# Kernel optimization log

Hardware: AMD Instinct MI355X
Metric: run time of the kernel (lower is better)

Reference implementation:

```python
import jax, jax.numpy as jnp
import numpy as np

B, N, C, H = 8, 784, 768, 16
HEAD_DIM = C // H
SCALE = HEAD_DIM ** -0.5


def rel_indices(num_patches):
    # ConViT relative position features: (dx, dy, dx^2+dy^2) per patch pair
    s = int(num_patches ** 0.5)
    ind = (jnp.arange(s)[None, :] - jnp.arange(s)[:, None]).astype(jnp.float32)
    indx = jnp.tile(ind, (s, s))                               # [N, N]
    indy = jnp.repeat(jnp.repeat(ind, s, axis=0), s, axis=1)   # [N, N]
    indd = indx ** 2 + indy ** 2
    return jnp.stack([indx, indy, indd], axis=-1)              # [N, N, 3]


def setup_inputs() -> dict:
    key = jax.random.key(0)
    ks = jax.random.split(key, 6)
    std = 0.02
    return {
        "x": jax.random.normal(ks[0], (B, N, C), dtype=jnp.float32),
        "Wq": jax.random.normal(ks[1], (C, C), dtype=jnp.float32) * std,
        "Wk": jax.random.normal(ks[2], (C, C), dtype=jnp.float32) * std,
        "Wv": jax.random.normal(ks[3], (C, C), dtype=jnp.float32) * std,
        "Wproj": jax.random.normal(ks[4], (C, C), dtype=jnp.float32) * std,
        "b_proj": jnp.zeros((C,), dtype=jnp.float32),
        "W_pos": jax.random.normal(ks[5], (H, 3), dtype=jnp.float32) * std,
        "b_pos": jnp.zeros((H,), dtype=jnp.float32),
        "gating": jnp.ones((H,), dtype=jnp.float32),
    }


def reference(x, Wq, Wk, Wv, Wproj, b_proj, W_pos, b_pos, gating):
    b, n, c = x.shape
    h, d = H, c // H

    def heads(W):
        # torch Linear: y = x @ W.T ; reshape to [b, h, n, d]
        return (x @ W.T).reshape(b, n, h, d).transpose(0, 2, 1, 3)

    q, k, v = heads(Wq), heads(Wk), heads(Wv)

    # content score: [b, h, n, n]
    patch_score = jnp.einsum('bhnd,bhmd->bhnm', q, k) * SCALE
    patch_score = jax.nn.softmax(patch_score, axis=-1)

    # positional score: rel [n,n,3] -> [h,n,n], broadcast over batch
    rel = rel_indices(n)
    pos_score = jnp.einsum('nmc,hc->hnm', rel, W_pos) + b_pos[:, None, None]
    pos_score = jax.nn.softmax(pos_score, axis=-1)

    g = jax.nn.sigmoid(gating)[None, :, None, None]  # [1,h,1,1]
    attn = (1.0 - g) * patch_score + g * pos_score[None]
    attn = attn / jnp.sum(attn, axis=-1, keepdims=True)

    out = jnp.einsum('bhnm,bhmd->bhnd', attn, v)
    out = out.transpose(0, 2, 1, 3).reshape(b, n, c)
    out = out @ Wproj.T + b_proj
    return out, attn, v
```

## Files before the change

### kernel.cpp

```cpp
#include <hip/hip_runtime.h>
#include <math.h>

#define BB 8
#define NN 784
#define CC 768
#define HH 16
#define DD 48
#define SCALE 0.14433756729740643f

#define ATTN_OFF ((size_t)BB*NN*CC)
#define V_OFF (ATTN_OFF + (size_t)BB*HH*NN*NN)

#define WS_XB ((size_t)0)
#define WS_WB ((size_t)4816896)
#define WS_QB (WS_WB + (size_t)4*589824)
#define WS_KB (WS_QB + (size_t)4816896)
#define WS_VT (WS_KB + (size_t)4816896)
#define WS_OB (WS_VT + (size_t)4816896)

using bf16x8 = __attribute__((ext_vector_type(8))) short;
using f32x4  = __attribute__((ext_vector_type(4))) float;

__device__ __forceinline__ short f2bf(float f) {
    union { float f; unsigned u; } uf; uf.f = f;
    unsigned u = uf.u;
    return (short)((u + 0x7FFFu + ((u >> 16) & 1u)) >> 16);
}
__device__ __forceinline__ bf16x8 bzero() {
    bf16x8 z = {0,0,0,0,0,0,0,0};
    return z;
}
__device__ __forceinline__ bf16x8 cvt8(float4 a, float4 b) {
    bf16x8 r;
    r[0]=f2bf(a.x); r[1]=f2bf(a.y); r[2]=f2bf(a.z); r[3]=f2bf(a.w);
    r[4]=f2bf(b.x); r[5]=f2bf(b.y); r[6]=f2bf(b.z); r[7]=f2bf(b.w);
    return r;
}
#define MFMA16(a,b,c) __builtin_amdgcn_mfma_f32_16x16x32_bf16((a),(b),(c),0,0,0)

__global__ __launch_bounds__(256) void cast_kernel(
    const float* __restrict__ x, const float* __restrict__ Wq,
    const float* __restrict__ Wk, const float* __restrict__ Wv,
    const float* __restrict__ Wp, short* __restrict__ xb, short* __restrict__ wb)
{
    int idx = blockIdx.x * 256 + threadIdx.x;
    const float* src;
    short* dst;
    if (idx < 1204224) {
        src = x + (size_t)idx * 4;
        dst = xb + (size_t)idx * 4;
    } else {
        int j = idx - 1204224;
        int sel = j / 147456;
        size_t off = (size_t)(j % 147456) * 4;
        const float* W = (sel == 0) ? Wq : (sel == 1) ? Wk : (sel == 2) ? Wv : Wp;
        src = W + off;
        dst = wb + (size_t)sel * 589824 + off;
    }
    float4 v = *(const float4*)src;
    union { short s[4]; uint2 u; } o;
    o.s[0] = f2bf(v.x); o.s[1] = f2bf(v.y); o.s[2] = f2bf(v.z); o.s[3] = f2bf(v.w);
    *(uint2*)dst = o.u;
}

__global__ __launch_bounds__(256) void qkv_mfma(
    const short* __restrict__ xb, const short* __restrict__ wb,
    short* __restrict__ qb, short* __restrict__ kb,
    float* __restrict__ vo, short* __restrict__ vt)
{
    const int t = threadIdx.x, l = t & 63, ww = t >> 6;
    const int quad = l >> 4, lc = l & 15;
    const int m0 = blockIdx.x * 128 + (ww >> 1) * 64;
    const int bn = blockIdx.y;
    const int wsel = bn / 6;
    const int colbase = (bn % 6) * 128 + (ww & 1) * 64;
    const short* W = wb + (size_t)wsel * 589824;

    f32x4 acc[4][4] = {};
    const short* arow = xb + (size_t)(m0 + lc) * 768 + quad * 8;
    const short* brow = W  + (size_t)(colbase + lc) * 768 + quad * 8;

    for (int k0 = 0; k0 < 768; k0 += 32) {
        bf16x8 af[4], bf[4];
#pragma unroll
        for (int i = 0; i < 4; i++) af[i] = *(const bf16x8*)(arow + (size_t)i * 16 * 768 + k0);
#pragma unroll
        for (int j = 0; j < 4; j++) bf[j] = *(const bf16x8*)(brow + (size_t)j * 16 * 768 + k0);
#pragma unroll
        for (int i = 0; i < 4; i++)
#pragma unroll
            for (int j = 0; j < 4; j++)
                acc[i][j] = MFMA16(af[i], bf[j], acc[i][j]);
    }

#pragma unroll
    for (int i = 0; i < 4; i++) {
#pragma unroll
        for (int j = 0; j < 4; j++) {
            const int o = colbase + j * 16 + lc;
            const int h = o / DD, d = o % DD;
#pragma unroll
            for (int r = 0; r < 4; r++) {
                const int m = m0 + i * 16 + quad * 4 + r;
                const int b = m / NN, n = m % NN;
                const size_t bhnd = (((size_t)b * HH + h) * NN + n) * DD + d;
                const float v = acc[i][j][r];
                if (wsel == 0)      qb[bhnd] = f2bf(v);
                else if (wsel == 1) kb[bhnd] = f2bf(v);
                else {
                    __builtin_nontemporal_store(v, vo + bhnd);
                    vt[((size_t)(b * HH + h) * DD + d) * NN + n] = f2bf(v);
                }
            }
        }
    }
}

__global__ __launch_bounds__(256) void attn_pv_fused(
    const short* __restrict__ qb, const short* __restrict__ kb,
    const short* __restrict__ vt,
    const float* __restrict__ W_pos, const float* __restrict__ b_pos,
    const float* __restrict__ gating, float* __restrict__ attn,
    short* __restrict__ ob)
{
    const int t = threadIdx.x, l = t & 63, ww = t >> 6;
    const int quad = l >> 4, lc = l & 15;
    const int bh = blockIdx.y, b = bh >> 4, h = bh & 15;
    const int row0 = blockIdx.x * 16;

    __shared__ __align__(16) float Sbuf[16][812];
    __shared__ float lxs[55], lys[55], fxs[55], fys[55];
    __shared__ float pmws[16][4];

    Sbuf[t >> 4][784 + (t & 15)] = 0.f;

    const short* qrow = qb + ((size_t)bh * NN + row0 + lc) * DD;
    bf16x8 qf0 = *(const bf16x8*)(qrow + quad * 8);
    bf16x8 qf1 = (quad < 2) ? *(const bf16x8*)(qrow + 32 + quad * 8) : bzero();

    float pmax[4] = {-3e38f, -3e38f, -3e38f, -3e38f};
    {
        int ct = ww;
        const short* krow = kb + ((size_t)bh * NN + ct * 16 + lc) * DD;
        bf16x8 kf0 = *(const bf16x8*)(krow + quad * 8);
        bf16x8 kf1 = (quad < 2) ? *(const bf16x8*)(krow + 32 + quad * 8) : bzero();
        while (ct < 49) {
            const int nct = ct + 4;
            bf16x8 nk0 = bzero(), nk1 = bzero();
            if (nct < 49) {
                const short* nrow = kb + ((size_t)bh * NN + nct * 16 + lc) * DD;
                nk0 = *(const bf16x8*)(nrow + quad * 8);
                nk1 = (quad < 2) ? *(const bf16x8*)(nrow + 32 + quad * 8) : bzero();
            }
            f32x4 cc = {0.f, 0.f, 0.f, 0.f};
            cc = MFMA16(qf0, kf0, cc);
            cc = MFMA16(qf1, kf1, cc);
            const int c0 = ct * 16;
#pragma unroll
            for (int r = 0; r < 4; r++) {
                Sbuf[quad * 4 + r][c0 + lc] = cc[r] * SCALE;
                pmax[r] = fmaxf(pmax[r], cc[r]);
            }
            kf0 = nk0; kf1 = nk1; ct = nct;
        }
    }
#pragma unroll
    for (int r = 0; r < 4; r++) {
        float v = pmax[r];
        v = fmaxf(v, __shfl_xor(v, 1));
        v = fmaxf(v, __shfl_xor(v, 2));
        v = fmaxf(v, __shfl_xor(v, 4));
        v = fmaxf(v, __shfl_xor(v, 8));
        if (lc == 0) pmws[quad * 4 + r][ww] = v;
    }

    const float w0 = W_pos[h * 3], w1 = W_pos[h * 3 + 1], w2 = W_pos[h * 3 + 2];
    if (t < 55) {
        const float d = (float)(t - 27);
        lxs[t] = fmaf(w2, d * d, w0 * d);
    } else if (t >= 64 && t < 119) {
        const float d = (float)(t - 91);
        lys[t - 64] = fmaf(w2, d * d, w1 * d);
    }

    __syncthreads();

    if (t < 55) {
        float m = lxs[0];
#pragma unroll
        for (int i = 1; i < 55; i++) m = fmaxf(m, lxs[i]);
        fxs[t] = __expf(lxs[t] - m);
    } else if (t >= 64 && t < 119) {
        float m = lys[0];
#pragma unroll
        for (int i = 1; i < 55; i++) m = fmaxf(m, lys[i]);
        fys[t - 64] = __expf(lys[t - 64] - m);
    }

    const int r = t >> 4, c = t & 15;
    const int nrow = row0 + r;
    const int nx = nrow % 28, ny = nrow / 28;

    const float sm = SCALE * fmaxf(fmaxf(pmws[r][0], pmws[r][1]),
                                   fmaxf(pmws[r][2], pmws[r][3]));
    float se = 0.f;
#pragma unroll 7
    for (int s = 0; s < 49; s++) {
        const float e = __expf(Sbuf[r][c + 16 * s] - sm);
        Sbuf[r][c + 16 * s] = e;
        se += e;
    }
    se += __shfl_xor(se, 1);
    se += __shfl_xor(se, 2);
    se += __shfl_xor(se, 4);
    se += __shfl_xor(se, 8);
    const float inv = 1.f / se;
    const float g = 1.f / (1.f + __expf(-gating[h]));

    __syncthreads();

    float Sx = 0.f, Sy = 0.f;
#pragma unroll
    for (int mx = 0; mx < 28; mx++) Sx += fxs[mx - nx + 27];
#pragma unroll
    for (int my = 0; my < 28; my++) Sy += fys[my - ny + 27];
    const float ginv = (1.f - g) * inv;
    const float gp = g / (Sx * Sy);

    float* arow = attn + ((size_t)bh * NN + nrow) * NN;
    {
        int mx = c, my = 0;
#pragma unroll 7
        for (int s = 0; s < 49; s++) {
            const int m = c + 16 * s;
            const float a = fmaf(Sbuf[r][m], ginv,
                                 fxs[mx - nx + 27] * fys[my - ny + 27] * gp);
            Sbuf[r][m] = a;
            __builtin_nontemporal_store(a, arow + m);
            mx += 16;
            if (mx >= 28) { mx -= 28; my++; }
        }
    }

    __syncthreads();

    const short* vbase = vt + (size_t)bh * DD * NN;
    f32x4 acc[3] = {};
    {
        const int kt0 = ww * 6;
        const int kt1 = (ww == 3) ? 25 : kt0 + 6;
        for (int kt = kt0; kt < kt1; kt++) {
            const int k0 = kt * 32 + quad * 8;
            float4 a0 = *(const float4*)&Sbuf[lc][k0];
            float4 a1 = *(const float4*)&Sbuf[lc][k0 + 4];
            bf16x8 af = cvt8(a0, a1);
#pragma unroll
            for (int j = 0; j < 3; j++) {
                bf16x8 bf = (k0 < NN)
                    ? *(const bf16x8*)(vbase + (size_t)(j * 16 + lc) * NN + k0)
                    : bzero();
                acc[j] = MFMA16(af, bf, acc[j]);
            }
        }
    }

    __syncthreads();

    float* Pacc = &Sbuf[0][0];
    if (ww > 0) {
#pragma unroll
        for (int j = 0; j < 3; j++)
            *(f32x4*)&Pacc[(((ww - 1) * 3 + j) * 64 + l) * 4] = acc[j];
    }

    __syncthreads();

    if (ww == 0) {
#pragma unroll
        for (int j = 0; j < 3; j++) {
#pragma unroll
            for (int w = 0; w < 3; w++)
                acc[j] += *(const f32x4*)&Pacc[((w * 3 + j) * 64 + l) * 4];
            const int d = h * DD + j * 16 + lc;
#pragma unroll
            for (int rr = 0; rr < 4; rr++) {
                const int rowi = row0 + quad * 4 + rr;
                ob[((size_t)b * NN + rowi) * CC + d] = f2bf(acc[j][rr]);
            }
        }
    }
}

__global__ __launch_bounds__(256) void proj_mfma(
    const short* __restrict__ ob, const short* __restrict__ wb,
    const float* __restrict__ bias, float* __restrict__ out)
{
    const int t = threadIdx.x, l = t & 63, ww = t >> 6;
    const int quad = l >> 4, lc = l & 15;
    const int m0 = blockIdx.x * 128 + (ww >> 1) * 64;
    const int colbase = blockIdx.y * 128 + (ww & 1) * 64;
    const short* W = wb + (size_t)3 * 589824;

    f32x4 acc[4][4] = {};
    const short* arow = ob + (size_t)(m0 + lc) * 768 + quad * 8;
    const short* brow = W  + (size_t)(colbase + lc) * 768 + quad * 8;

    for (int k0 = 0; k0 < 768; k0 += 32) {
        bf16x8 af[4], bf[4];
#pragma unroll
        for (int i = 0; i < 4; i++) af[i] = *(const bf16x8*)(arow + (size_t)i * 16 * 768 + k0);
#pragma unroll
        for (int j = 0; j < 4; j++) bf[j] = *(const bf16x8*)(brow + (size_t)j * 16 * 768 + k0);
#pragma unroll
        for (int i = 0; i < 4; i++)
#pragma unroll
            for (int j = 0; j < 4; j++)
                acc[i][j] = MFMA16(af[i], bf[j], acc[i][j]);
    }

#pragma unroll
    for (int i = 0; i < 4; i++) {
#pragma unroll
        for (int j = 0; j < 4; j++) {
            const int o = colbase + j * 16 + lc;
            const float bo = bias[o];
#pragma unroll
            for (int r = 0; r < 4; r++) {
                const int m = m0 + i * 16 + quad * 4 + r;
                __builtin_nontemporal_store(acc[i][j][r] + bo, out + (size_t)m * CC + o);
            }
        }
    }
}

extern "C" void kernel_launch(void* const* d_in, const int* in_sizes, int n_in,
                              void* d_out, int out_size, void* d_ws, size_t ws_size,
                              hipStream_t stream)
{
    const float* x      = (const float*)d_in[0];
    const float* Wq     = (const float*)d_in[1];
    const float* Wk     = (const float*)d_in[2];
    const float* Wv     = (const float*)d_in[3];
    const float* Wproj  = (const float*)d_in[4];
    const float* b_proj = (const float*)d_in[5];
    const float* W_pos  = (const float*)d_in[6];
    const float* b_pos  = (const float*)d_in[7];
    const float* gating = (const float*)d_in[8];

    float* out  = (float*)d_out;
    short* ws   = (short*)d_ws;

    short* xb = ws + WS_XB;
    short* wb = ws + WS_WB;
    short* qb = ws + WS_QB;
    short* kb = ws + WS_KB;
    short* vt = ws + WS_VT;
    short* ob = ws + WS_OB;
    float* attn = out + ATTN_OFF;
    float* vout = out + V_OFF;

    hipLaunchKernelGGL(cast_kernel, dim3(7008), dim3(256), 0, stream,
                       x, Wq, Wk, Wv, Wproj, xb, wb);
    hipLaunchKernelGGL(qkv_mfma, dim3(49, 18), dim3(256), 0, stream,
                       xb, wb, qb, kb, vout, vt);
    hipLaunchKernelGGL(attn_pv_fused, dim3(49, 128), dim3(256), 0, stream,
                       qb, kb, vt, W_pos, b_pos, gating, attn, ob);
    hipLaunchKernelGGL(proj_mfma, dim3(49, 6), dim3(256), 0, stream,
                       ob, wb, b_proj, out);
}
```

Baseline: 638.3 us.

## Remap block IDs per XCD for L2 locality and vectorize softmax/blend LDS access

Flattens the grids of the QKV GEMM, fused attention and projection kernels to 1D and remaps block indices so consecutive logical tiles land on the same XCD. Blocks sharing K/V or weight tiles then reuse the same L2. It also rewrites the exp and blend loops in the attention kernel to work on float4 chunks, so each thread handles contiguous columns and issues 128-bit LDS accesses and attn stores instead of scalar strided ones. The remap assumes the hardware assigns blocks to the 8 XCDs round-robin, and the blend now does more integer index work per element.

```diff
diff --git a/kernel.cpp b/kernel.cpp
--- a/kernel.cpp
+++ b/kernel.cpp
@@ -30,10 +30,10 @@
     bf16x8 z = {0,0,0,0,0,0,0,0};
     return z;
 }
-__device__ __forceinline__ bf16x8 cvt8(float4 a, float4 b) {
+__device__ __forceinline__ bf16x8 cvt8v(f32x4 a, f32x4 b) {
     bf16x8 r;
-    r[0]=f2bf(a.x); r[1]=f2bf(a.y); r[2]=f2bf(a.z); r[3]=f2bf(a.w);
-    r[4]=f2bf(b.x); r[5]=f2bf(b.y); r[6]=f2bf(b.z); r[7]=f2bf(b.w);
+    r[0]=f2bf(a[0]); r[1]=f2bf(a[1]); r[2]=f2bf(a[2]); r[3]=f2bf(a[3]);
+    r[4]=f2bf(b[0]); r[5]=f2bf(b[1]); r[6]=f2bf(b[2]); r[7]=f2bf(b[3]);
     return r;
 }
 #define MFMA16(a,b,c) __builtin_amdgcn_mfma_f32_16x16x32_bf16((a),(b),(c),0,0,0)
@@ -57,9 +57,9 @@
         src = W + off;
         dst = wb + (size_t)sel * 589824 + off;
     }
-    float4 v = *(const float4*)src;
+    f32x4 v = *(const f32x4*)src;
     union { short s[4]; uint2 u; } o;
-    o.s[0] = f2bf(v.x); o.s[1] = f2bf(v.y); o.s[2] = f2bf(v.z); o.s[3] = f2bf(v.w);
+    o.s[0] = f2bf(v[0]); o.s[1] = f2bf(v[1]); o.s[2] = f2bf(v[2]); o.s[3] = f2bf(v[3]);
     *(uint2*)dst = o.u;
 }
 
@@ -70,8 +70,12 @@
 {
     const int t = threadIdx.x, l = t & 63, ww = t >> 6;
     const int quad = l >> 4, lc = l & 15;
-    const int m0 = blockIdx.x * 128 + (ww >> 1) * 64;
-    const int bn = blockIdx.y;
+    const int P = blockIdx.x, xcd = P & 7, ii = P >> 3;
+    const int start = (xcd < 2) ? xcd * 111 : 222 + (xcd - 2) * 110;
+    const int orig = start + ii;
+    const int bx = orig / 18, bn = orig % 18;
+
+    const int m0 = bx * 128 + (ww >> 1) * 64;
     const int wsel = bn / 6;
     const int colbase = (bn % 6) * 128 + (ww & 1) * 64;
     const short* W = wb + (size_t)wsel * 589824;
@@ -125,8 +129,10 @@
 {
     const int t = threadIdx.x, l = t & 63, ww = t >> 6;
     const int quad = l >> 4, lc = l & 15;
-    const int bh = blockIdx.y, b = bh >> 4, h = bh & 15;
-    const int row0 = blockIdx.x * 16;
+    const int P = blockIdx.x;
+    const int orig = (P & 7) * 784 + (P >> 3);
+    const int bh = orig / 49, b = bh >> 4, h = bh & 15;
+    const int row0 = (orig % 49) * 16;
 
     __shared__ __align__(16) float Sbuf[16][812];
     __shared__ float lxs[55], lys[55], fxs[55], fys[55];
@@ -204,11 +210,20 @@
     const float sm = SCALE * fmaxf(fmaxf(pmws[r][0], pmws[r][1]),
                                    fmaxf(pmws[r][2], pmws[r][3]));
     float se = 0.f;
-#pragma unroll 7
-    for (int s = 0; s < 49; s++) {
-        const float e = __expf(Sbuf[r][c + 16 * s] - sm);
-        Sbuf[r][c + 16 * s] = e;
-        se += e;
+#pragma unroll 4
+    for (int s = 0; s < 12; s++) {
+        f32x4 v = *(const f32x4*)&Sbuf[r][c * 4 + 64 * s];
+        v[0] = __expf(v[0] - sm); v[1] = __expf(v[1] - sm);
+        v[2] = __expf(v[2] - sm); v[3] = __expf(v[3] - sm);
+        *(f32x4*)&Sbuf[r][c * 4 + 64 * s] = v;
+        se += (v[0] + v[1]) + (v[2] + v[3]);
+    }
+    if (c < 4) {
+        f32x4 v = *(const f32x4*)&Sbuf[r][768 + c * 4];
+        v[0] = __expf(v[0] - sm); v[1] = __expf(v[1] - sm);
+        v[2] = __expf(v[2] - sm); v[3] = __expf(v[3] - sm);
+        *(f32x4*)&Sbuf[r][768 + c * 4] = v;
+        se += (v[0] + v[1]) + (v[2] + v[3]);
     }
     se += __shfl_xor(se, 1);
     se += __shfl_xor(se, 2);
@@ -228,19 +243,28 @@
     const float gp = g / (Sx * Sy);
 
     float* arow = attn + ((size_t)bh * NN + nrow) * NN;
-    {
-        int mx = c, my = 0;
-#pragma unroll 7
-        for (int s = 0; s < 49; s++) {
-            const int m = c + 16 * s;
-            const float a = fmaf(Sbuf[r][m], ginv,
-                                 fxs[mx - nx + 27] * fys[my - ny + 27] * gp);
-            Sbuf[r][m] = a;
-            __builtin_nontemporal_store(a, arow + m);
-            mx += 16;
-            if (mx >= 28) { mx -= 28; my++; }
-        }
-    }
+    const float* fxp = fxs + 27 - nx;
+    const float* fyp = fys + 27 - ny;
+#define BLEND4(M0)                                                         \
+    {                                                                      \
+        const int m0_ = (M0);                                              \
+        f32x4 v = *(const f32x4*)&Sbuf[r][m0_];                            \
+        int mx = m0_ % 28, my = m0_ / 28;                                  \
+        f32x4 a;                                                           \
+        a[0] = fmaf(v[0], ginv, fxp[mx] * fyp[my] * gp);                   \
+        if (++mx == 28) { mx = 0; my++; }                                  \
+        a[1] = fmaf(v[1], ginv, fxp[mx] * fyp[my] * gp);                   \
+        if (++mx == 28) { mx = 0; my++; }                                  \
+        a[2] = fmaf(v[2], ginv, fxp[mx] * fyp[my] * gp);                   \
+        if (++mx == 28) { mx = 0; my++; }                                  \
+        a[3] = fmaf(v[3], ginv, fxp[mx] * fyp[my] * gp);                   \
+        *(f32x4*)&Sbuf[r][m0_] = a;                                        \
+        __builtin_nontemporal_store(a, (f32x4*)(arow + m0_));              \
+    }
+#pragma unroll 4
+    for (int s = 0; s < 12; s++) BLEND4(c * 4 + 64 * s);
+    if (c < 4) BLEND4(768 + c * 4);
+#undef BLEND4
 
     __syncthreads();
 
@@ -251,9 +275,9 @@
         const int kt1 = (ww == 3) ? 25 : kt0 + 6;
         for (int kt = kt0; kt < kt1; kt++) {
             const int k0 = kt * 32 + quad * 8;
-            float4 a0 = *(const float4*)&Sbuf[lc][k0];
-            float4 a1 = *(const float4*)&Sbuf[lc][k0 + 4];
-            bf16x8 af = cvt8(a0, a1);
+            f32x4 a0 = *(const f32x4*)&Sbuf[lc][k0];
+            f32x4 a1 = *(const f32x4*)&Sbuf[lc][k0 + 4];
+            bf16x8 af = cvt8v(a0, a1);
 #pragma unroll
             for (int j = 0; j < 3; j++) {
                 bf16x8 bf = (k0 < NN)
@@ -297,8 +321,13 @@
 {
     const int t = threadIdx.x, l = t & 63, ww = t >> 6;
     const int quad = l >> 4, lc = l & 15;
-    const int m0 = blockIdx.x * 128 + (ww >> 1) * 64;
-    const int colbase = blockIdx.y * 128 + (ww & 1) * 64;
+    const int P = blockIdx.x, xcd = P & 7, ii = P >> 3;
+    const int start = (xcd < 6) ? xcd * 37 : 222 + (xcd - 6) * 36;
+    const int orig = start + ii;
+    const int bx = orig / 6, by = orig % 6;
+
+    const int m0 = bx * 128 + (ww >> 1) * 64;
+    const int colbase = by * 128 + (ww & 1) * 64;
     const short* W = wb + (size_t)3 * 589824;
 
     f32x4 acc[4][4] = {};
@@ -361,10 +390,10 @@
 
     hipLaunchKernelGGL(cast_kernel, dim3(7008), dim3(256), 0, stream,
                        x, Wq, Wk, Wv, Wproj, xb, wb);
-    hipLaunchKernelGGL(qkv_mfma, dim3(49, 18), dim3(256), 0, stream,
+    hipLaunchKernelGGL(qkv_mfma, dim3(882), dim3(256), 0, stream,
                        xb, wb, qb, kb, vout, vt);
-    hipLaunchKernelGGL(attn_pv_fused, dim3(49, 128), dim3(256), 0, stream,
+    hipLaunchKernelGGL(attn_pv_fused, dim3(6272), dim3(256), 0, stream,
                        qb, kb, vt, W_pos, b_pos, gating, attn, ob);
-    hipLaunchKernelGGL(proj_mfma, dim3(49, 6), dim3(256), 0, stream,
+    hipLaunchKernelGGL(proj_mfma, dim3(294), dim3(256), 0, stream,
                        ob, wb, b_proj, out);
 }
```

New measurement: 629.0 us. Within noise of the previous version (-1.5%).
